# Optimization experiments

Measured on AMD Instinct MI355X. Metric: run time of the kernel, lower is better.

## Reference

```python
import jax, jax.numpy as jnp
import numpy as np

D_IN = 1024
D_OUT = 1024
NUM_HEADS = 16
HEAD_DIM = D_OUT // NUM_HEADS


def setup_inputs() -> dict:
    key = jax.random.key(0)
    ks = jax.random.split(key, 6)
    s = 1.0 / np.sqrt(D_IN)
    return {
        "x": jax.random.normal(ks[0], (4, 2048, D_IN), dtype=jnp.float32),
        "Wq": jax.random.uniform(ks[1], (D_IN, D_OUT), jnp.float32, -s, s),
        "Wk": jax.random.uniform(ks[2], (D_IN, D_OUT), jnp.float32, -s, s),
        "Wv": jax.random.uniform(ks[3], (D_IN, D_OUT), jnp.float32, -s, s),
        "Wo": jax.random.uniform(ks[4], (D_OUT, D_OUT), jnp.float32, -s, s),
        "bo": jax.random.uniform(ks[5], (D_OUT,), jnp.float32, -s, s),
    }


def reference(x, Wq, Wk, Wv, Wo, bo):
    b, n, _ = x.shape
    # QKV projections -> [b, h, n, d]
    def heads(t):
        return t.reshape(b, n, NUM_HEADS, HEAD_DIM).transpose(0, 2, 1, 3)
    q = heads(x @ Wq)
    k = heads(x @ Wk)
    v = heads(x @ Wv)
    # scaled scores with causal mask
    scores = jnp.einsum("bhqd,bhkd->bhqk", q, k) / jnp.sqrt(jnp.float32(HEAD_DIM))
    causal = jnp.tril(jnp.ones((n, n), dtype=bool))  # True = keep
    scores = jnp.where(causal, scores, -jnp.inf)
    attn = jax.nn.softmax(scores, axis=-1)  # dropout p=0.0 -> identity
    ctx = jnp.einsum("bhqk,bhkd->bhqd", attn, v)
    ctx = ctx.transpose(0, 2, 1, 3).reshape(b, n, D_OUT)
    return ctx @ Wo + bo
```

## Files before the change

### kernel.cpp

```cpp
#include <hip/hip_runtime.h>
#include <hip/hip_bf16.h>
#include <math.h>

typedef __attribute__((ext_vector_type(8))) __bf16 bf16x8;
typedef __attribute__((ext_vector_type(4))) __bf16 bf16x4;
typedef __attribute__((ext_vector_type(4))) float f32x4;
typedef __attribute__((ext_vector_type(4))) short short4_t;

#define D_MODEL 1024
#define SEQ     2048
#define BATCH   4
#define NH      16
#define HD      64
#define MROWS   (BATCH * SEQ)

#define SCALE_LOG2E 0.18033688011112042f

__device__ __forceinline__ void gld_lds16(const __bf16* g, __bf16* l) {
  __builtin_amdgcn_global_load_lds(
      (const __attribute__((address_space(1))) void*)g,
      (__attribute__((address_space(3))) void*)l, 16, 0, 0);
}

__global__ __launch_bounds__(256) void cvt_x(const float* __restrict__ in,
                                             __bf16* __restrict__ out) {
  int i = (blockIdx.x * 256 + threadIdx.x) * 4;
  float4 f = *(const float4*)(in + i);
  bf16x4 o;
  o.x = (__bf16)f.x; o.y = (__bf16)f.y; o.z = (__bf16)f.z; o.w = (__bf16)f.w;
  *(bf16x4*)(out + i) = o;
}

__global__ __launch_bounds__(256) void cvt_wt(const float* __restrict__ W,
                                              __bf16* __restrict__ Wt) {
  __shared__ __bf16 t[32][33];
  int tx = threadIdx.x, ty = threadIdx.y;
  int n0 = blockIdx.x * 32, k0 = blockIdx.y * 32;
#pragma unroll
  for (int j = 0; j < 32; j += 8)
    t[ty + j][tx] = (__bf16)W[(size_t)(k0 + ty + j) * D_MODEL + n0 + tx];
  __syncthreads();
#pragma unroll
  for (int j = 0; j < 32; j += 8)
    Wt[(size_t)(n0 + ty + j) * D_MODEL + k0 + tx] = t[tx][ty + j];
}

template <int EPI>
__global__ __launch_bounds__(256) void gemm_bt(const __bf16* __restrict__ A,
                                               const __bf16* __restrict__ Bt,
                                               const float* __restrict__ bias,
                                               void* __restrict__ Cout) {
  constexpr int Kd = 1024;
  constexpr bool SWAP = (EPI != 1);
  __shared__ __bf16 As[128 * 32];
  __shared__ __bf16 Bs[128 * 32];
  const int tid = threadIdx.x;
  const int lane = tid & 63;
  const int w = tid >> 6;
  const int quad = lane >> 4, l16 = lane & 15;
  const int wr = w >> 1, wc = w & 1;
  const int tm = blockIdx.y * 128, tn = blockIdx.x * 128;

  f32x4 acc[4][4] = {};

  const int u0 = (w * 2) * 64 + lane;
  const int u1 = u0 + 64;
  const int rA0 = u0 >> 2, kofs0 = (u0 & 3) * 8;
  const int rA1 = u1 >> 2, kofs1 = (u1 & 3) * 8;
  const __bf16* gA0 = A + (size_t)(tm + rA0) * Kd + kofs0;
  const __bf16* gA1 = A + (size_t)(tm + rA1) * Kd + kofs1;
  const __bf16* gB0 = Bt + (size_t)(tn + rA0) * Kd + kofs0;
  const __bf16* gB1 = Bt + (size_t)(tn + rA1) * Kd + kofs1;
  __bf16* lA0 = As + (w * 2 + 0) * 512;
  __bf16* lA1 = As + (w * 2 + 1) * 512;
  __bf16* lB0 = Bs + (w * 2 + 0) * 512;
  __bf16* lB1 = Bs + (w * 2 + 1) * 512;

  for (int k0 = 0; k0 < Kd; k0 += 32) {
    gld_lds16(gA0 + k0, lA0);
    gld_lds16(gA1 + k0, lA1);
    gld_lds16(gB0 + k0, lB0);
    gld_lds16(gB1 + k0, lB1);
    __syncthreads();
    bf16x8 af[4], bfr[4];
#pragma unroll
    for (int t = 0; t < 4; ++t) {
      af[t]  = *(const bf16x8*)&As[(wr * 64 + t * 16 + l16) * 32 + quad * 8];
      bfr[t] = *(const bf16x8*)&Bs[(wc * 64 + t * 16 + l16) * 32 + quad * 8];
    }
#pragma unroll
    for (int mt = 0; mt < 4; ++mt)
#pragma unroll
      for (int nt = 0; nt < 4; ++nt) {
        if constexpr (SWAP)
          acc[mt][nt] = __builtin_amdgcn_mfma_f32_16x16x32_bf16(
              bfr[nt], af[mt], acc[mt][nt], 0, 0, 0);
        else
          acc[mt][nt] = __builtin_amdgcn_mfma_f32_16x16x32_bf16(
              af[mt], bfr[nt], acc[mt][nt], 0, 0, 0);
      }
    __syncthreads();
  }

#pragma unroll
  for (int mt = 0; mt < 4; ++mt)
#pragma unroll
    for (int nt = 0; nt < 4; ++nt) {
      if constexpr (EPI == 2) {
        int gm  = tm + wr * 64 + mt * 16 + l16;
        int gn0 = tn + wc * 64 + nt * 16 + quad * 4;
        float4 bv = *(const float4*)&bias[gn0];
        float4 o;
        o.x = acc[mt][nt][0] + bv.x;
        o.y = acc[mt][nt][1] + bv.y;
        o.z = acc[mt][nt][2] + bv.z;
        o.w = acc[mt][nt][3] + bv.w;
        *(float4*)&((float*)Cout)[(size_t)gm * 1024 + gn0] = o;
      } else if constexpr (EPI == 0) {
        int gm = tm + wr * 64 + mt * 16 + l16;
        int f0 = tn + wc * 64 + nt * 16 + quad * 4;
        int which = f0 >> 10, col = f0 & 1023;
        int b = gm >> 11, nn = gm & 2047, h = col >> 6, d = col & 63;
        float s = (which == 0) ? SCALE_LOG2E : 1.0f;
        bf16x4 o;
        o[0] = (__bf16)(acc[mt][nt][0] * s);
        o[1] = (__bf16)(acc[mt][nt][1] * s);
        o[2] = (__bf16)(acc[mt][nt][2] * s);
        o[3] = (__bf16)(acc[mt][nt][3] * s);
        __bf16* op = (__bf16*)Cout + (size_t)which * (BATCH * SEQ * (size_t)D_MODEL) +
                     ((size_t)(b * NH + h) * SEQ + nn) * HD + d;
        *(bf16x4*)op = o;
      } else {
        int gm0 = tm + wr * 64 + mt * 16 + quad * 4;
        int gn  = tn + wc * 64 + nt * 16 + l16;
        int b = gm0 >> 11, nn0 = gm0 & 2047, h = gn >> 6, d = gn & 63;
        bf16x4 o;
        o[0] = (__bf16)acc[mt][nt][0];
        o[1] = (__bf16)acc[mt][nt][1];
        o[2] = (__bf16)acc[mt][nt][2];
        o[3] = (__bf16)acc[mt][nt][3];
        __bf16* op = (__bf16*)Cout + ((size_t)(b * NH + h) * HD + d) * SEQ + nn0;
        *(bf16x4*)op = o;
      }
    }
}

__global__ __launch_bounds__(256, 2) void attn(const __bf16* __restrict__ Q,
                                               const __bf16* __restrict__ K,
                                               const __bf16* __restrict__ Vt,
                                               __bf16* __restrict__ ctx) {
  const int tid = threadIdx.x;
  const int lane = tid & 63, w = tid >> 6;
  const int quad = lane >> 4, l16 = lane & 15;
  const int pr = blockIdx.x;
  const int bh = blockIdx.y;
  const int tile0 = pr, tile1 = 15 - pr;
  const __bf16* qb = Q + (size_t)bh * SEQ * HD;
  const __bf16* kb = K + (size_t)bh * SEQ * HD;
  const __bf16* vb = Vt + (size_t)bh * HD * SEQ;

  __shared__ __bf16 KsAll[2 * 4096];
  __shared__ __bf16 VsAll[2 * 4096];

  const int qmin[2] = {tile0 * 128 + w * 32, tile1 * 128 + w * 32};

  bf16x8 aq[2][2][2];
#pragma unroll
  for (int p = 0; p < 2; ++p)
#pragma unroll
    for (int qq = 0; qq < 2; ++qq)
#pragma unroll
      for (int kk = 0; kk < 2; ++kk)
        aq[p][qq][kk] = *(const bf16x8*)(qb + (size_t)(qmin[p] + qq * 16 + l16) * HD +
                                         kk * 32 + quad * 8);

  f32x4 acc[2][2][4] = {};
  float lsum[2][2] = {};

  const int u0 = w * 128 + lane;
  const int u1 = u0 + 64;
  const int kOffG0 = ((u0 >> 2) & 63) * HD + (u0 >> 8) * 32 + (u0 & 3) * 8;
  const int kOffG1 = ((u1 >> 2) & 63) * HD + (u1 >> 8) * 32 + (u1 & 3) * 8;
  const int vd0 = u0 >> 3, vd1 = u1 >> 3;
  const int vOffG0 = vd0 * SEQ + (((u0 & 7) ^ (vd0 & 7)) * 8);
  const int vOffG1 = vd1 * SEQ + (((u1 & 7) ^ (vd1 & 7)) * 8);

  auto stage = [&](int k0s, int bufsel) {
    __bf16* Kb = KsAll + bufsel * 4096;
    __bf16* Vb = VsAll + bufsel * 4096;
    gld_lds16(kb + (size_t)k0s * HD + kOffG0, Kb + u0 * 8);
    gld_lds16(kb + (size_t)k0s * HD + kOffG1, Kb + u1 * 8);
    gld_lds16(vb + k0s + vOffG0, Vb + u0 * 8);
    gld_lds16(vb + k0s + vOffG1, Vb + u1 * 8);
  };

  const int nIter = 2 * tile1 + 2;
  stage(0, 0);

  for (int it = 0; it < nIter; ++it) {
    __syncthreads();
    if (it + 1 < nIter) stage((it + 1) * 64, (it + 1) & 1);

    const int k0 = it * 64;
    if (k0 <= qmin[1] + 31) {
      const __bf16* Kb = KsAll + (it & 1) * 4096;
      const __bf16* Vb = VsAll + (it & 1) * 4096;

      bf16x8 bk[4][2];
#pragma unroll
      for (int kt = 0; kt < 4; ++kt)
#pragma unroll
        for (int kk = 0; kk < 2; ++kk)
          bk[kt][kk] = *(const bf16x8*)&Kb[kk * 2048 + (kt * 16 + l16) * 32 + quad * 8];

      short4_t vf[4][4];
#pragma unroll
      for (int kt = 0; kt < 4; ++kt)
#pragma unroll
        for (int cd = 0; cd < 4; ++cd)
          vf[kt][cd] = *(const short4_t*)&Vb[(cd * 16 + l16) * 64 +
                                             (((kt * 2 + (quad >> 1)) ^ (l16 & 7)) * 8) +
                                             (quad & 1) * 4];

#pragma unroll
      for (int p = 0; p < 2; ++p) {
        if (k0 > qmin[p] + 31) continue;
        f32x4 St[4][2] = {};
#pragma unroll
        for (int kt = 0; kt < 4; ++kt)
#pragma unroll
          for (int qq = 0; qq < 2; ++qq) {
            St[kt][qq] = __builtin_amdgcn_mfma_f32_16x16x32_bf16(
                bk[kt][0], aq[p][qq][0], St[kt][qq], 0, 0, 0);
            St[kt][qq] = __builtin_amdgcn_mfma_f32_16x16x32_bf16(
                bk[kt][1], aq[p][qq][1], St[kt][qq], 0, 0, 0);
          }
        const bool full = (k0 + 63 <= qmin[p]);
#pragma unroll
        for (int kt = 0; kt < 4; ++kt)
#pragma unroll
          for (int qq = 0; qq < 2; ++qq) {
            float e0 = __builtin_amdgcn_exp2f(St[kt][qq][0]);
            float e1 = __builtin_amdgcn_exp2f(St[kt][qq][1]);
            float e2 = __builtin_amdgcn_exp2f(St[kt][qq][2]);
            float e3 = __builtin_amdgcn_exp2f(St[kt][qq][3]);
            if (!full) {
              int kg = k0 + kt * 16 + quad * 4;
              int qg = qmin[p] + qq * 16 + l16;
              if (kg + 0 > qg) e0 = 0.f;
              if (kg + 1 > qg) e1 = 0.f;
              if (kg + 2 > qg) e2 = 0.f;
              if (kg + 3 > qg) e3 = 0.f;
            }
            lsum[p][qq] += (e0 + e1) + (e2 + e3);
            short4_t ap;
            ap[0] = __builtin_bit_cast(short, (__bf16)e0);
            ap[1] = __builtin_bit_cast(short, (__bf16)e1);
            ap[2] = __builtin_bit_cast(short, (__bf16)e2);
            ap[3] = __builtin_bit_cast(short, (__bf16)e3);
#pragma unroll
            for (int cd = 0; cd < 4; ++cd)
              acc[p][qq][cd] = __builtin_amdgcn_mfma_f32_16x16x16bf16_1k(
                  ap, vf[kt][cd], acc[p][qq][cd], 0, 0, 0);
          }
      }
    }
  }

  const int bb = bh >> 4, hh = bh & 15;
#pragma unroll
  for (int p = 0; p < 2; ++p) {
#pragma unroll
    for (int qq = 0; qq < 2; ++qq) {
      float s = lsum[p][qq];
      s += __shfl_xor(s, 16);
      s += __shfl_xor(s, 32);
      float rinv[4];
#pragma unroll
      for (int i = 0; i < 4; ++i)
        rinv[i] = 1.0f / __shfl(s, (lane & 48) + quad * 4 + i);
#pragma unroll
      for (int c = 0; c < 4; ++c)
#pragma unroll
        for (int i = 0; i < 4; ++i) {
          int q = qmin[p] + qq * 16 + quad * 4 + i;
          float o = acc[p][qq][c][i] * rinv[i];
          ctx[((size_t)(bb * SEQ + q)) * D_MODEL + hh * HD + c * 16 + l16] = (__bf16)o;
        }
    }
  }
}

extern "C" void kernel_launch(void* const* d_in, const int* in_sizes, int n_in,
                              void* d_out, int out_size, void* d_ws, size_t ws_size,
                              hipStream_t stream) {
  const float* x  = (const float*)d_in[0];
  const float* Wq = (const float*)d_in[1];
  const float* Wk = (const float*)d_in[2];
  const float* Wv = (const float*)d_in[3];
  const float* Wo = (const float*)d_in[4];
  const float* bo = (const float*)d_in[5];
  float* out = (float*)d_out;
  char* ws = (char*)d_ws;
  const size_t MB = 1024 * 1024;
  __bf16* xb   = (__bf16*)(ws);
  __bf16* Wqkv = (__bf16*)(ws + 16 * MB);
  __bf16* Wot  = (__bf16*)(ws + 22 * MB);
  __bf16* Qh   = (__bf16*)(ws + 24 * MB);
  __bf16* Kh   = (__bf16*)(ws + 40 * MB);
  __bf16* Vth  = (__bf16*)(ws + 56 * MB);
  __bf16* ctx  = xb;

  cvt_x<<<MROWS * D_MODEL / (256 * 4), 256, 0, stream>>>(x, xb);
  dim3 tb(32, 8);
  cvt_wt<<<dim3(32, 32), tb, 0, stream>>>(Wq, Wqkv);
  cvt_wt<<<dim3(32, 32), tb, 0, stream>>>(Wk, Wqkv + 1024 * 1024);
  cvt_wt<<<dim3(32, 32), tb, 0, stream>>>(Wv, Wqkv + 2 * 1024 * 1024);
  cvt_wt<<<dim3(32, 32), tb, 0, stream>>>(Wo, Wot);

  gemm_bt<0><<<dim3(16, 64), 256, 0, stream>>>(xb, Wqkv, nullptr, Qh);
  gemm_bt<1><<<dim3(8, 64), 256, 0, stream>>>(xb, Wqkv + 2 * 1024 * 1024, nullptr, Vth);

  attn<<<dim3(8, BATCH * NH), 256, 0, stream>>>(Qh, Kh, Vth, ctx);

  gemm_bt<2><<<dim3(8, 64), 256, 0, stream>>>(ctx, Wot, bo, out);
}
```

Before: 272.3 us.

## Split attention across 8 waves of 16 query rows with MFMA row sums

```diff
diff --git a/kernel.cpp b/kernel.cpp
--- a/kernel.cpp
+++ b/kernel.cpp
@@ -145,7 +145,7 @@
     }
 }
 
-__global__ __launch_bounds__(256, 2) void attn(const __bf16* __restrict__ Q,
+__global__ __launch_bounds__(512, 4) void attn(const __bf16* __restrict__ Q,
                                                const __bf16* __restrict__ K,
                                                const __bf16* __restrict__ Vt,
                                                __bf16* __restrict__ ctx) {
@@ -162,36 +162,31 @@
   __shared__ __bf16 KsAll[2 * 4096];
   __shared__ __bf16 VsAll[2 * 4096];
 
-  const int qmin[2] = {tile0 * 128 + w * 32, tile1 * 128 + w * 32};
-
-  bf16x8 aq[2][2][2];
+  const int qmin[2] = {tile0 * 128 + w * 16, tile1 * 128 + w * 16};
+
+  bf16x8 aq[2][2];
 #pragma unroll
   for (int p = 0; p < 2; ++p)
 #pragma unroll
-    for (int qq = 0; qq < 2; ++qq)
-#pragma unroll
-      for (int kk = 0; kk < 2; ++kk)
-        aq[p][qq][kk] = *(const bf16x8*)(qb + (size_t)(qmin[p] + qq * 16 + l16) * HD +
-                                         kk * 32 + quad * 8);
-
-  f32x4 acc[2][2][4] = {};
-  float lsum[2][2] = {};
-
-  const int u0 = w * 128 + lane;
-  const int u1 = u0 + 64;
-  const int kOffG0 = ((u0 >> 2) & 63) * HD + (u0 >> 8) * 32 + (u0 & 3) * 8;
-  const int kOffG1 = ((u1 >> 2) & 63) * HD + (u1 >> 8) * 32 + (u1 & 3) * 8;
-  const int vd0 = u0 >> 3, vd1 = u1 >> 3;
-  const int vOffG0 = vd0 * SEQ + (((u0 & 7) ^ (vd0 & 7)) * 8);
-  const int vOffG1 = vd1 * SEQ + (((u1 & 7) ^ (vd1 & 7)) * 8);
+    for (int kk = 0; kk < 2; ++kk)
+      aq[p][kk] = *(const bf16x8*)(qb + (size_t)(qmin[p] + l16) * HD +
+                                   kk * 32 + quad * 8);
+
+  f32x4 acc[2][4] = {};
+  f32x4 accs[2] = {};
+
+  const short4_t ones = {0x3F80, 0x3F80, 0x3F80, 0x3F80};
+
+  const int u = tid;
+  const int kOffG = ((u >> 2) & 63) * HD + (u >> 8) * 32 + (u & 3) * 8;
+  const int vd = u >> 3;
+  const int vOffG = vd * SEQ + (((u & 7) ^ (vd & 7)) * 8);
 
   auto stage = [&](int k0s, int bufsel) {
     __bf16* Kb = KsAll + bufsel * 4096;
     __bf16* Vb = VsAll + bufsel * 4096;
-    gld_lds16(kb + (size_t)k0s * HD + kOffG0, Kb + u0 * 8);
-    gld_lds16(kb + (size_t)k0s * HD + kOffG1, Kb + u1 * 8);
-    gld_lds16(vb + k0s + vOffG0, Vb + u0 * 8);
-    gld_lds16(vb + k0s + vOffG1, Vb + u1 * 8);
+    gld_lds16(kb + (size_t)k0s * HD + kOffG, Kb + u * 8);
+    gld_lds16(vb + k0s + vOffG, Vb + u * 8);
   };
 
   const int nIter = 2 * tile1 + 2;
@@ -202,7 +197,7 @@
     if (it + 1 < nIter) stage((it + 1) * 64, (it + 1) & 1);
 
     const int k0 = it * 64;
-    if (k0 <= qmin[1] + 31) {
+    if (k0 <= qmin[1] + 15) {
       const __bf16* Kb = KsAll + (it & 1) * 4096;
       const __bf16* Vb = VsAll + (it & 1) * 4096;
 
@@ -224,45 +219,42 @@
 
 #pragma unroll
       for (int p = 0; p < 2; ++p) {
-        if (k0 > qmin[p] + 31) continue;
-        f32x4 St[4][2] = {};
-#pragma unroll
-        for (int kt = 0; kt < 4; ++kt)
-#pragma unroll
-          for (int qq = 0; qq < 2; ++qq) {
-            St[kt][qq] = __builtin_amdgcn_mfma_f32_16x16x32_bf16(
-                bk[kt][0], aq[p][qq][0], St[kt][qq], 0, 0, 0);
-            St[kt][qq] = __builtin_amdgcn_mfma_f32_16x16x32_bf16(
-                bk[kt][1], aq[p][qq][1], St[kt][qq], 0, 0, 0);
+        if (k0 > qmin[p] + 15) continue;
+        f32x4 St[4] = {};
+#pragma unroll
+        for (int kt = 0; kt < 4; ++kt) {
+          St[kt] = __builtin_amdgcn_mfma_f32_16x16x32_bf16(
+              bk[kt][0], aq[p][0], St[kt], 0, 0, 0);
+          St[kt] = __builtin_amdgcn_mfma_f32_16x16x32_bf16(
+              bk[kt][1], aq[p][1], St[kt], 0, 0, 0);
+        }
+        const bool full = (k0 + 63 <= qmin[p]);
+#pragma unroll
+        for (int kt = 0; kt < 4; ++kt) {
+          float e0 = __builtin_amdgcn_exp2f(St[kt][0]);
+          float e1 = __builtin_amdgcn_exp2f(St[kt][1]);
+          float e2 = __builtin_amdgcn_exp2f(St[kt][2]);
+          float e3 = __builtin_amdgcn_exp2f(St[kt][3]);
+          if (!full) {
+            int kg = k0 + kt * 16 + quad * 4;
+            int qg = qmin[p] + l16;
+            if (kg + 0 > qg) e0 = 0.f;
+            if (kg + 1 > qg) e1 = 0.f;
+            if (kg + 2 > qg) e2 = 0.f;
+            if (kg + 3 > qg) e3 = 0.f;
           }
-        const bool full = (k0 + 63 <= qmin[p]);
-#pragma unroll
-        for (int kt = 0; kt < 4; ++kt)
-#pragma unroll
-          for (int qq = 0; qq < 2; ++qq) {
-            float e0 = __builtin_amdgcn_exp2f(St[kt][qq][0]);
-            float e1 = __builtin_amdgcn_exp2f(St[kt][qq][1]);
-            float e2 = __builtin_amdgcn_exp2f(St[kt][qq][2]);
-            float e3 = __builtin_amdgcn_exp2f(St[kt][qq][3]);
-            if (!full) {
-              int kg = k0 + kt * 16 + quad * 4;
-              int qg = qmin[p] + qq * 16 + l16;
-              if (kg + 0 > qg) e0 = 0.f;
-              if (kg + 1 > qg) e1 = 0.f;
-              if (kg + 2 > qg) e2 = 0.f;
-              if (kg + 3 > qg) e3 = 0.f;
-            }
-            lsum[p][qq] += (e0 + e1) + (e2 + e3);
-            short4_t ap;
-            ap[0] = __builtin_bit_cast(short, (__bf16)e0);
-            ap[1] = __builtin_bit_cast(short, (__bf16)e1);
-            ap[2] = __builtin_bit_cast(short, (__bf16)e2);
-            ap[3] = __builtin_bit_cast(short, (__bf16)e3);
-#pragma unroll
-            for (int cd = 0; cd < 4; ++cd)
-              acc[p][qq][cd] = __builtin_amdgcn_mfma_f32_16x16x16bf16_1k(
-                  ap, vf[kt][cd], acc[p][qq][cd], 0, 0, 0);
-          }
+          short4_t ap;
+          ap[0] = __builtin_bit_cast(short, (__bf16)e0);
+          ap[1] = __builtin_bit_cast(short, (__bf16)e1);
+          ap[2] = __builtin_bit_cast(short, (__bf16)e2);
+          ap[3] = __builtin_bit_cast(short, (__bf16)e3);
+          accs[p] = __builtin_amdgcn_mfma_f32_16x16x16bf16_1k(
+              ap, ones, accs[p], 0, 0, 0);
+#pragma unroll
+          for (int cd = 0; cd < 4; ++cd)
+            acc[p][cd] = __builtin_amdgcn_mfma_f32_16x16x16bf16_1k(
+                vf[kt][cd], ap, acc[p][cd], 0, 0, 0);
+        }
       }
     }
   }
@@ -270,23 +262,24 @@
   const int bb = bh >> 4, hh = bh & 15;
 #pragma unroll
   for (int p = 0; p < 2; ++p) {
-#pragma unroll
-    for (int qq = 0; qq < 2; ++qq) {
-      float s = lsum[p][qq];
-      s += __shfl_xor(s, 16);
-      s += __shfl_xor(s, 32);
-      float rinv[4];
-#pragma unroll
-      for (int i = 0; i < 4; ++i)
-        rinv[i] = 1.0f / __shfl(s, (lane & 48) + quad * 4 + i);
-#pragma unroll
-      for (int c = 0; c < 4; ++c)
-#pragma unroll
-        for (int i = 0; i < 4; ++i) {
-          int q = qmin[p] + qq * 16 + quad * 4 + i;
-          float o = acc[p][qq][c][i] * rinv[i];
-          ctx[((size_t)(bb * SEQ + q)) * D_MODEL + hh * HD + c * 16 + l16] = (__bf16)o;
-        }
+    float sv[4];
+#pragma unroll
+    for (int i = 0; i < 4; ++i)
+      sv[i] = __shfl(accs[p][i], (l16 >> 2) * 16);
+    float s01 = (l16 & 1) ? sv[1] : sv[0];
+    float s23 = (l16 & 1) ? sv[3] : sv[2];
+    float rinv = 1.0f / ((l16 & 2) ? s23 : s01);
+
+    const int q = qmin[p] + l16;
+    __bf16* orow = ctx + ((size_t)(bb * SEQ + q)) * D_MODEL + hh * HD;
+#pragma unroll
+    for (int cd = 0; cd < 4; ++cd) {
+      bf16x4 o;
+      o[0] = (__bf16)(acc[p][cd][0] * rinv);
+      o[1] = (__bf16)(acc[p][cd][1] * rinv);
+      o[2] = (__bf16)(acc[p][cd][2] * rinv);
+      o[3] = (__bf16)(acc[p][cd][3] * rinv);
+      *(bf16x4*)(orow + cd * 16 + quad * 4) = o;
     }
   }
 }
@@ -321,7 +314,7 @@
   gemm_bt<0><<<dim3(16, 64), 256, 0, stream>>>(xb, Wqkv, nullptr, Qh);
   gemm_bt<1><<<dim3(8, 64), 256, 0, stream>>>(xb, Wqkv + 2 * 1024 * 1024, nullptr, Vth);
 
-  attn<<<dim3(8, BATCH * NH), 256, 0, stream>>>(Qh, Kh, Vth, ctx);
+  attn<<<dim3(8, BATCH * NH), 512, 0, stream>>>(Qh, Kh, Vth, ctx);
 
   gemm_bt<2><<<dim3(8, 64), 256, 0, stream>>>(ctx, Wot, bo, out);
 }
```

Result: slower. 443.2 us (+62.8%).
